# Performance work log

Hardware: AMD Instinct MI355X
Metric: run time of the kernel (lower is better)

Reference implementation:

```python
import jax, jax.numpy as jnp
import numpy as np

E, CAP, S, H, I, K = 160, 120, 3200, 2048, 192, 6  # experts, capacity, seq, hidden, per-device ffn dim, top-k


def setup_inputs() -> dict:
    key = jax.random.key(0)
    ks = jax.random.split(key, 8)
    hidden_states = jax.random.normal(ks[0], (S, H), jnp.float32)
    token_index = jax.random.randint(ks[1], (E, CAP), 0, S, dtype=jnp.int32)
    # re_index is a permutation mapping concatenated per-expert outputs back to (topk, seq) order
    re_index = jax.random.permutation(ks[2], E * CAP).astype(jnp.int32)
    topk_weight = jax.random.uniform(ks[3], (K, S, 1), jnp.float32)
    shared_out = jax.random.normal(ks[4], (1, S, H), jnp.float32)
    scale = 0.02
    gate_w = jax.random.normal(ks[5], (E, I, H), jnp.float32) * scale
    up_w = jax.random.normal(ks[6], (E, I, H), jnp.float32) * scale
    down_w = jax.random.normal(ks[7], (E, H, I), jnp.float32) * scale
    return {
        "hidden_states": hidden_states,
        "token_index": token_index,
        "re_index": re_index,
        "topk_weight": topk_weight,
        "shared_out": shared_out,
        "gate_w": gate_w,
        "up_w": up_w,
        "down_w": down_w,
    }


def reference(hidden_states, token_index, re_index, topk_weight, shared_out, gate_w, up_w, down_w):
    # Gather per-expert token groups: [E, CAP, H]
    x = hidden_states[token_index]
    # SwiGLU expert FFN, batched over all experts (grouped GEMM)
    g = jnp.einsum('ech,eih->eci', x, gate_w)   # [E, CAP, I]
    u = jnp.einsum('ech,eih->eci', x, up_w)     # [E, CAP, I]
    h = jax.nn.silu(g) * u
    o = jnp.einsum('eci,ehi->ech', h, down_w)   # [E, CAP, H]
    # Scatter back into (topk, seq) layout and combine with routing weights
    flat = o.reshape(E * CAP, H)[re_index].reshape(K, S, H)
    out = (flat * topk_weight).sum(axis=0, keepdims=True) + shared_out  # [1, S, H]
    return out
```

## Files before the change

### kernel.cpp

```cpp
#include <hip/hip_runtime.h>
#include <hip/hip_bf16.h>

#define E_ 160
#define CAP_ 120
#define S_ 3200
#define H_ 2048
#define I_ 192
#define K_ 6
#define MP_ 128

typedef __attribute__((ext_vector_type(8))) short short8;
typedef __attribute__((ext_vector_type(4))) float f32x4;

__device__ __forceinline__ unsigned pack2bf(float a, float b) {
  return __builtin_amdgcn_perm(__float_as_uint(b), __float_as_uint(a), 0x07060302u);
}
__device__ __forceinline__ short f2bf1(float a) {
  return (short)(__float_as_uint(a) >> 16);
}
__device__ __forceinline__ float bf2f(short s) {
  return __uint_as_float(((unsigned)(unsigned short)s) << 16);
}

__global__ __launch_bounds__(256) void k_gather(
    const float* __restrict__ hidden, const int* __restrict__ tok,
    short* __restrict__ xb)
{
  int b = blockIdx.x;
  int e = b >> 7, c = b & 127;
  int col = threadIdx.x * 8;
  short* dst = xb + (size_t)b * H_ + col;
  if (c < CAP_) {
    int row = tok[e * CAP_ + c];
    const float* src = hidden + (size_t)row * H_ + col;
    float4 f0 = *(const float4*)src;
    float4 f1 = *(const float4*)(src + 4);
    int4 v;
    v.x = (int)pack2bf(f0.x, f0.y); v.y = (int)pack2bf(f0.z, f0.w);
    v.z = (int)pack2bf(f1.x, f1.y); v.w = (int)pack2bf(f1.z, f1.w);
    *(int4*)dst = v;
  } else {
    *(int4*)dst = make_int4(0, 0, 0, 0);
  }
}

__global__ __launch_bounds__(256) void k_gateup(
    const short* __restrict__ xb, const float* __restrict__ gw,
    const float* __restrict__ uw, short* __restrict__ hb)
{
  __shared__ __align__(16) char smem[34816];
  short* As = (short*)smem;
  short* Bs = As + 128 * 64;

  int bid = blockIdx.x;
  int e = bid / 3, t = bid - e * 3;
  int i0 = t * 64;
  int tid = threadIdx.x;
  int lane = tid & 63, w = tid >> 6;
  int wr = w >> 1, wc = w & 1;
  int lrow = lane & 15, lq = lane >> 4;

  f32x4 acc[4][4] = {};
  const size_t xbase = (size_t)e * MP_ * H_;

  for (int kk = 0; kk < H_ / 64; ++kk) {
    int k0 = kk * 64;
#pragma unroll
    for (int r = 0; r < 4; ++r) {
      int q = r * 256 + tid;
      int row = q >> 3, cc = q & 7;
      int4 v = *(const int4*)(xb + xbase + (size_t)row * H_ + k0 + cc * 8);
      *(int4*)(As + row * 64 + cc * 8) = v;
    }
#pragma unroll
    for (int r = 0; r < 8; ++r) {
      int p = r * 256 + tid;
      int row = p >> 4, cc = p & 15;
      const float* srcw = (row < 64)
          ? (gw + ((size_t)e * I_ + i0 + row) * H_ + k0 + cc * 4)
          : (uw + ((size_t)e * I_ + i0 + row - 64) * H_ + k0 + cc * 4);
      float4 f = *(const float4*)srcw;
      uint2 pv;
      pv.x = pack2bf(f.x, f.y); pv.y = pack2bf(f.z, f.w);
      *(uint2*)(Bs + row * 64 + cc * 4) = pv;
    }
    __syncthreads();
#pragma unroll
    for (int ks = 0; ks < 2; ++ks) {
      int koff = ks * 32 + lq * 8;
      short8 a[4], bb[4];
#pragma unroll
      for (int tr = 0; tr < 4; ++tr)
        a[tr] = *(const short8*)(As + (wr * 64 + tr * 16 + lrow) * 64 + koff);
#pragma unroll
      for (int tc = 0; tc < 4; ++tc)
        bb[tc] = *(const short8*)(Bs + (wc * 64 + tc * 16 + lrow) * 64 + koff);
#pragma unroll
      for (int tr = 0; tr < 4; ++tr)
#pragma unroll
        for (int tc = 0; tc < 4; ++tc)
          acc[tr][tc] = __builtin_amdgcn_mfma_f32_16x16x32_bf16(
              a[tr], bb[tc], acc[tr][tc], 0, 0, 0);
    }
    __syncthreads();
  }

  float* exch = (float*)smem;
  if (wc == 0) {
#pragma unroll
    for (int tr = 0; tr < 4; ++tr)
#pragma unroll
      for (int tc = 0; tc < 4; ++tc)
#pragma unroll
        for (int rg = 0; rg < 4; ++rg) {
          int lr = tr * 16 + lq * 4 + rg;
          int lcol = tc * 16 + lrow;
          exch[(wr * 64 + lr) * 68 + lcol] = acc[tr][tc][rg];
        }
  }
  __syncthreads();
  if (wc == 1) {
#pragma unroll
    for (int tr = 0; tr < 4; ++tr)
#pragma unroll
      for (int tc = 0; tc < 4; ++tc)
#pragma unroll
        for (int rg = 0; rg < 4; ++rg) {
          int lr = tr * 16 + lq * 4 + rg;
          int lcol = tc * 16 + lrow;
          float g = exch[(wr * 64 + lr) * 68 + lcol];
          float u = acc[tr][tc][rg];
          float hv = g / (1.f + __expf(-g)) * u;
          hb[((size_t)e * MP_ + wr * 64 + lr) * I_ + i0 + lcol] = f2bf1(hv);
        }
  }
}

__global__ __launch_bounds__(256) void k_down(
    const short* __restrict__ hb, const float* __restrict__ dw,
    short* __restrict__ ob)
{
  __shared__ __align__(16) short As[128 * 64];
  __shared__ __align__(16) short Bs[128 * 64];
  int bid = blockIdx.x;
  int e = bid >> 4, t = bid & 15;
  int n0 = t * 128;
  int tid = threadIdx.x;
  int lane = tid & 63, w = tid >> 6;
  int wr = w >> 1, wc = w & 1;
  int lrow = lane & 15, lq = lane >> 4;

  f32x4 acc[4][4] = {};

  for (int kk = 0; kk < 3; ++kk) {
    int k0 = kk * 64;
#pragma unroll
    for (int r = 0; r < 4; ++r) {
      int q = r * 256 + tid;
      int row = q >> 3, cc = q & 7;
      int4 v = *(const int4*)(hb + ((size_t)e * MP_ + row) * I_ + k0 + cc * 8);
      *(int4*)(As + row * 64 + cc * 8) = v;
    }
#pragma unroll
    for (int r = 0; r < 8; ++r) {
      int p = r * 256 + tid;
      int row = p >> 4, cc = p & 15;
      const float* srcw = dw + ((size_t)e * H_ + n0 + row) * I_ + k0 + cc * 4;
      float4 f = *(const float4*)srcw;
      uint2 pv;
      pv.x = pack2bf(f.x, f.y); pv.y = pack2bf(f.z, f.w);
      *(uint2*)(Bs + row * 64 + cc * 4) = pv;
    }
    __syncthreads();
#pragma unroll
    for (int ks = 0; ks < 2; ++ks) {
      int koff = ks * 32 + lq * 8;
      short8 a[4], bb[4];
#pragma unroll
      for (int tr = 0; tr < 4; ++tr)
        a[tr] = *(const short8*)(As + (wr * 64 + tr * 16 + lrow) * 64 + koff);
#pragma unroll
      for (int tc = 0; tc < 4; ++tc)
        bb[tc] = *(const short8*)(Bs + (wc * 64 + tc * 16 + lrow) * 64 + koff);
#pragma unroll
      for (int tr = 0; tr < 4; ++tr)
#pragma unroll
        for (int tc = 0; tc < 4; ++tc)
          acc[tr][tc] = __builtin_amdgcn_mfma_f32_16x16x32_bf16(
              a[tr], bb[tc], acc[tr][tc], 0, 0, 0);
    }
    __syncthreads();
  }

#pragma unroll
  for (int tr = 0; tr < 4; ++tr) {
#pragma unroll
    for (int rg = 0; rg < 4; ++rg) {
      int c = wr * 64 + tr * 16 + lq * 4 + rg;
      if (c < CAP_) {
#pragma unroll
        for (int tc = 0; tc < 4; ++tc) {
          int col = n0 + wc * 64 + tc * 16 + lrow;
          ob[((size_t)e * CAP_ + c) * H_ + col] = f2bf1(acc[tr][tc][rg]);
        }
      }
    }
  }
}

__global__ __launch_bounds__(256) void k_combine(
    const short* __restrict__ ob, const int* __restrict__ re_index,
    const float* __restrict__ topk, const float* __restrict__ shared_out,
    float* __restrict__ out)
{
  int s = blockIdx.x;
  int c0 = threadIdx.x * 8;
  const float* sh = shared_out + (size_t)s * H_ + c0;
  float4 s0 = *(const float4*)sh;
  float4 s1 = *(const float4*)(sh + 4);
  float r[8] = {s0.x, s0.y, s0.z, s0.w, s1.x, s1.y, s1.z, s1.w};
#pragma unroll
  for (int k = 0; k < K_; ++k) {
    int p = k * S_ + s;
    int idx = re_index[p];
    float wgt = topk[p];
    const short* row = ob + (size_t)idx * H_ + c0;
    short8 v = *(const short8*)row;
#pragma unroll
    for (int j = 0; j < 8; ++j) r[j] += wgt * bf2f(v[j]);
  }
  float* o = out + (size_t)s * H_ + c0;
  float4 o0, o1;
  o0.x = r[0]; o0.y = r[1]; o0.z = r[2]; o0.w = r[3];
  o1.x = r[4]; o1.y = r[5]; o1.z = r[6]; o1.w = r[7];
  *(float4*)o = o0;
  *(float4*)(o + 4) = o1;
}

extern "C" void kernel_launch(void* const* d_in, const int* in_sizes, int n_in,
                              void* d_out, int out_size, void* d_ws, size_t ws_size,
                              hipStream_t stream) {
  const float* hidden     = (const float*)d_in[0];
  const int*   tok        = (const int*)d_in[1];
  const int*   re_index   = (const int*)d_in[2];
  const float* topk       = (const float*)d_in[3];
  const float* shared_out = (const float*)d_in[4];
  const float* gw         = (const float*)d_in[5];
  const float* uw         = (const float*)d_in[6];
  const float* dw         = (const float*)d_in[7];
  float* out = (float*)d_out;

  char* ws = (char*)d_ws;
  short* xb = (short*)ws;
  short* hb = (short*)(ws + (size_t)E_ * MP_ * H_ * 2);
  short* ob = (short*)(ws + (size_t)E_ * MP_ * H_ * 2
                          + (size_t)E_ * MP_ * I_ * 2);

  hipLaunchKernelGGL(k_gather,  dim3(E_ * MP_), dim3(256), 0, stream, hidden, tok, xb);
  hipLaunchKernelGGL(k_gateup,  dim3(E_ * 3),   dim3(256), 0, stream, xb, gw, uw, hb);
  hipLaunchKernelGGL(k_down,    dim3(E_ * 16),  dim3(256), 0, stream, hb, dw, ob);
  hipLaunchKernelGGL(k_combine, dim3(S_),       dim3(256), 0, stream, ob, re_index, topk, shared_out, out);
}
```

Baseline: 738.2 us.

## Fuse token gather into gate/up GEMM with register prefetch and swizzled LDS

Removes the separate gather kernel so the gate/up GEMM reads hidden rows directly by token index and converts them to bf16 on the fly. The gate/up tile is split along M (64 rows), doubling the grid to 960 blocks. Global loads for the next K step are prefetched into registers while the current step computes. Both GEMMs now use an XOR-swizzled LDS layout to reduce bank conflicts. The cost is that each weight tile is converted twice (once per M half) and hidden rows are re-read per i-tile.

```diff
diff --git a/kernel.cpp b/kernel.cpp
--- a/kernel.cpp
+++ b/kernel.cpp
@@ -21,117 +21,152 @@
 __device__ __forceinline__ float bf2f(short s) {
   return __uint_as_float(((unsigned)(unsigned short)s) << 16);
 }
-
-__global__ __launch_bounds__(256) void k_gather(
+__device__ __forceinline__ int4 pack8(float4 lo, float4 hi) {
+  int4 v;
+  v.x = (int)pack2bf(lo.x, lo.y); v.y = (int)pack2bf(lo.z, lo.w);
+  v.z = (int)pack2bf(hi.x, hi.y); v.w = (int)pack2bf(hi.z, hi.w);
+  return v;
+}
+
+#define NI_GU (H_ / 64)
+__global__ __launch_bounds__(256) void k_gateup(
     const float* __restrict__ hidden, const int* __restrict__ tok,
-    short* __restrict__ xb)
+    const float* __restrict__ gw, const float* __restrict__ uw,
+    short* __restrict__ hb)
 {
-  int b = blockIdx.x;
-  int e = b >> 7, c = b & 127;
-  int col = threadIdx.x * 8;
-  short* dst = xb + (size_t)b * H_ + col;
-  if (c < CAP_) {
-    int row = tok[e * CAP_ + c];
-    const float* src = hidden + (size_t)row * H_ + col;
-    float4 f0 = *(const float4*)src;
-    float4 f1 = *(const float4*)(src + 4);
-    int4 v;
-    v.x = (int)pack2bf(f0.x, f0.y); v.y = (int)pack2bf(f0.z, f0.w);
-    v.z = (int)pack2bf(f1.x, f1.y); v.w = (int)pack2bf(f1.z, f1.w);
-    *(int4*)dst = v;
-  } else {
-    *(int4*)dst = make_int4(0, 0, 0, 0);
-  }
-}
-
-__global__ __launch_bounds__(256) void k_gateup(
-    const short* __restrict__ xb, const float* __restrict__ gw,
-    const float* __restrict__ uw, short* __restrict__ hb)
-{
-  __shared__ __align__(16) char smem[34816];
+  __shared__ __align__(16) char smem[(64 * 64 + 128 * 64) * 2];
   short* As = (short*)smem;
-  short* Bs = As + 128 * 64;
+  short* Bs = As + 64 * 64;
 
   int bid = blockIdx.x;
-  int e = bid / 3, t = bid - e * 3;
-  int i0 = t * 64;
+  int e = bid / 6;
+  int r6 = bid - e * 6;
+  int it = r6 >> 1, mt = r6 & 1;
+  int i0 = it * 64, m0 = mt * 64;
   int tid = threadIdx.x;
   int lane = tid & 63, w = tid >> 6;
   int wr = w >> 1, wc = w & 1;
   int lrow = lane & 15, lq = lane >> 4;
 
-  f32x4 acc[4][4] = {};
-  const size_t xbase = (size_t)e * MP_ * H_;
-
-  for (int kk = 0; kk < H_ / 64; ++kk) {
-    int k0 = kk * 64;
-#pragma unroll
-    for (int r = 0; r < 4; ++r) {
-      int q = r * 256 + tid;
-      int row = q >> 3, cc = q & 7;
-      int4 v = *(const int4*)(xb + xbase + (size_t)row * H_ + k0 + cc * 8);
-      *(int4*)(As + row * 64 + cc * 8) = v;
-    }
-#pragma unroll
-    for (int r = 0; r < 8; ++r) {
-      int p = r * 256 + tid;
-      int row = p >> 4, cc = p & 15;
-      const float* srcw = (row < 64)
-          ? (gw + ((size_t)e * I_ + i0 + row) * H_ + k0 + cc * 4)
-          : (uw + ((size_t)e * I_ + i0 + row - 64) * H_ + k0 + cc * 4);
-      float4 f = *(const float4*)srcw;
-      uint2 pv;
-      pv.x = pack2bf(f.x, f.y); pv.y = pack2bf(f.z, f.w);
-      *(uint2*)(Bs + row * 64 + cc * 4) = pv;
-    }
-    __syncthreads();
+  const float* aptr[2]; int aphys[2];
+#pragma unroll
+  for (int q = 0; q < 2; ++q) {
+    int c = q * 256 + tid;
+    int arow = c >> 3, jc = c & 7;
+    int tr_ = m0 + arow; if (tr_ > CAP_ - 1) tr_ = CAP_ - 1;
+    int tokrow = tok[e * CAP_ + tr_];
+    aptr[q] = hidden + (size_t)tokrow * H_ + jc * 8;
+    aphys[q] = arow * 8 + (jc ^ (arow & 7));
+  }
+  const float* bptr[4]; int bphys[4];
+#pragma unroll
+  for (int q = 0; q < 4; ++q) {
+    int c = q * 256 + tid;
+    int brow = c >> 3, jc = c & 7;
+    const float* base = (brow < 64)
+        ? gw + ((size_t)e * I_ + i0 + brow) * H_
+        : uw + ((size_t)e * I_ + i0 + brow - 64) * H_;
+    bptr[q] = base + jc * 8;
+    bphys[q] = brow * 8 + (jc ^ (brow & 7));
+  }
+
+  f32x4 acc[2][4] = {};
+  float4 apre[2][2], bpre[4][2];
+
+#pragma unroll
+  for (int q = 0; q < 2; ++q) {
+    apre[q][0] = *(const float4*)(aptr[q]);
+    apre[q][1] = *(const float4*)(aptr[q] + 4);
+  }
+#pragma unroll
+  for (int q = 0; q < 4; ++q) {
+    bpre[q][0] = *(const float4*)(bptr[q]);
+    bpre[q][1] = *(const float4*)(bptr[q] + 4);
+  }
+#pragma unroll
+  for (int q = 0; q < 2; ++q)
+    *(int4*)(As + aphys[q] * 8) = pack8(apre[q][0], apre[q][1]);
+#pragma unroll
+  for (int q = 0; q < 4; ++q)
+    *(int4*)(Bs + bphys[q] * 8) = pack8(bpre[q][0], bpre[q][1]);
+  __syncthreads();
+
+  for (int kk = 0; kk < NI_GU; ++kk) {
+    bool hasNext = (kk + 1) < NI_GU;
+    if (hasNext) {
+      int k0 = (kk + 1) * 64;
+#pragma unroll
+      for (int q = 0; q < 2; ++q) {
+        apre[q][0] = *(const float4*)(aptr[q] + k0);
+        apre[q][1] = *(const float4*)(aptr[q] + k0 + 4);
+      }
+#pragma unroll
+      for (int q = 0; q < 4; ++q) {
+        bpre[q][0] = *(const float4*)(bptr[q] + k0);
+        bpre[q][1] = *(const float4*)(bptr[q] + k0 + 4);
+      }
+    }
 #pragma unroll
     for (int ks = 0; ks < 2; ++ks) {
-      int koff = ks * 32 + lq * 8;
-      short8 a[4], bb[4];
-#pragma unroll
-      for (int tr = 0; tr < 4; ++tr)
-        a[tr] = *(const short8*)(As + (wr * 64 + tr * 16 + lrow) * 64 + koff);
-#pragma unroll
-      for (int tc = 0; tc < 4; ++tc)
-        bb[tc] = *(const short8*)(Bs + (wc * 64 + tc * 16 + lrow) * 64 + koff);
-#pragma unroll
-      for (int tr = 0; tr < 4; ++tr)
+      short8 a[2], bb[4];
+#pragma unroll
+      for (int tr = 0; tr < 2; ++tr) {
+        int m = wr * 32 + tr * 16 + lrow;
+        int jc = ks * 4 + lq;
+        a[tr] = *(const short8*)(As + (m * 8 + (jc ^ (m & 7))) * 8);
+      }
+#pragma unroll
+      for (int tc = 0; tc < 4; ++tc) {
+        int n = wc * 64 + tc * 16 + lrow;
+        int jc = ks * 4 + lq;
+        bb[tc] = *(const short8*)(Bs + (n * 8 + (jc ^ (n & 7))) * 8);
+      }
+#pragma unroll
+      for (int tr = 0; tr < 2; ++tr)
 #pragma unroll
         for (int tc = 0; tc < 4; ++tc)
           acc[tr][tc] = __builtin_amdgcn_mfma_f32_16x16x32_bf16(
               a[tr], bb[tc], acc[tr][tc], 0, 0, 0);
     }
     __syncthreads();
+    if (hasNext) {
+#pragma unroll
+      for (int q = 0; q < 2; ++q)
+        *(int4*)(As + aphys[q] * 8) = pack8(apre[q][0], apre[q][1]);
+#pragma unroll
+      for (int q = 0; q < 4; ++q)
+        *(int4*)(Bs + bphys[q] * 8) = pack8(bpre[q][0], bpre[q][1]);
+    }
+    __syncthreads();
   }
 
   float* exch = (float*)smem;
   if (wc == 0) {
 #pragma unroll
-    for (int tr = 0; tr < 4; ++tr)
+    for (int tr = 0; tr < 2; ++tr)
 #pragma unroll
       for (int tc = 0; tc < 4; ++tc)
 #pragma unroll
         for (int rg = 0; rg < 4; ++rg) {
-          int lr = tr * 16 + lq * 4 + rg;
-          int lcol = tc * 16 + lrow;
-          exch[(wr * 64 + lr) * 68 + lcol] = acc[tr][tc][rg];
+          int row = wr * 32 + tr * 16 + lq * 4 + rg;
+          int col = tc * 16 + lrow;
+          exch[row * 68 + col] = acc[tr][tc][rg];
         }
   }
   __syncthreads();
   if (wc == 1) {
 #pragma unroll
-    for (int tr = 0; tr < 4; ++tr)
+    for (int tr = 0; tr < 2; ++tr)
 #pragma unroll
       for (int tc = 0; tc < 4; ++tc)
 #pragma unroll
         for (int rg = 0; rg < 4; ++rg) {
-          int lr = tr * 16 + lq * 4 + rg;
-          int lcol = tc * 16 + lrow;
-          float g = exch[(wr * 64 + lr) * 68 + lcol];
+          int row = wr * 32 + tr * 16 + lq * 4 + rg;
+          int col = tc * 16 + lrow;
+          float g = exch[row * 68 + col];
           float u = acc[tr][tc][rg];
           float hv = g / (1.f + __expf(-g)) * u;
-          hb[((size_t)e * MP_ + wr * 64 + lr) * I_ + i0 + lcol] = f2bf1(hv);
+          hb[((size_t)e * MP_ + m0 + row) * I_ + i0 + col] = f2bf1(hv);
         }
   }
 }
@@ -155,33 +190,37 @@
   for (int kk = 0; kk < 3; ++kk) {
     int k0 = kk * 64;
 #pragma unroll
-    for (int r = 0; r < 4; ++r) {
-      int q = r * 256 + tid;
-      int row = q >> 3, cc = q & 7;
-      int4 v = *(const int4*)(hb + ((size_t)e * MP_ + row) * I_ + k0 + cc * 8);
-      *(int4*)(As + row * 64 + cc * 8) = v;
-    }
-#pragma unroll
-    for (int r = 0; r < 8; ++r) {
-      int p = r * 256 + tid;
-      int row = p >> 4, cc = p & 15;
-      const float* srcw = dw + ((size_t)e * H_ + n0 + row) * I_ + k0 + cc * 4;
-      float4 f = *(const float4*)srcw;
-      uint2 pv;
-      pv.x = pack2bf(f.x, f.y); pv.y = pack2bf(f.z, f.w);
-      *(uint2*)(Bs + row * 64 + cc * 4) = pv;
+    for (int q = 0; q < 4; ++q) {
+      int c = q * 256 + tid;
+      int arow = c >> 3, jc = c & 7;
+      int4 v = *(const int4*)(hb + ((size_t)e * MP_ + arow) * I_ + k0 + jc * 8);
+      *(int4*)(As + (arow * 8 + (jc ^ (arow & 7))) * 8) = v;
+    }
+#pragma unroll
+    for (int q = 0; q < 4; ++q) {
+      int c = q * 256 + tid;
+      int brow = c >> 3, jc = c & 7;
+      const float* src = dw + ((size_t)e * H_ + n0 + brow) * I_ + k0 + jc * 8;
+      float4 lo = *(const float4*)src;
+      float4 hi = *(const float4*)(src + 4);
+      *(int4*)(Bs + (brow * 8 + (jc ^ (brow & 7))) * 8) = pack8(lo, hi);
     }
     __syncthreads();
 #pragma unroll
     for (int ks = 0; ks < 2; ++ks) {
-      int koff = ks * 32 + lq * 8;
       short8 a[4], bb[4];
 #pragma unroll
-      for (int tr = 0; tr < 4; ++tr)
-        a[tr] = *(const short8*)(As + (wr * 64 + tr * 16 + lrow) * 64 + koff);
-#pragma unroll
-      for (int tc = 0; tc < 4; ++tc)
-        bb[tc] = *(const short8*)(Bs + (wc * 64 + tc * 16 + lrow) * 64 + koff);
+      for (int tr = 0; tr < 4; ++tr) {
+        int m = wr * 64 + tr * 16 + lrow;
+        int jc = ks * 4 + lq;
+        a[tr] = *(const short8*)(As + (m * 8 + (jc ^ (m & 7))) * 8);
+      }
+#pragma unroll
+      for (int tc = 0; tc < 4; ++tc) {
+        int n = wc * 64 + tc * 16 + lrow;
+        int jc = ks * 4 + lq;
+        bb[tc] = *(const short8*)(Bs + (n * 8 + (jc ^ (n & 7))) * 8);
+      }
 #pragma unroll
       for (int tr = 0; tr < 4; ++tr)
 #pragma unroll
@@ -251,13 +290,12 @@
   float* out = (float*)d_out;
 
   char* ws = (char*)d_ws;
-  short* xb = (short*)ws;
-  short* hb = (short*)(ws + (size_t)E_ * MP_ * H_ * 2);
-  short* ob = (short*)(ws + (size_t)E_ * MP_ * H_ * 2
-                          + (size_t)E_ * MP_ * I_ * 2);
-
-  hipLaunchKernelGGL(k_gather,  dim3(E_ * MP_), dim3(256), 0, stream, hidden, tok, xb);
-  hipLaunchKernelGGL(k_gateup,  dim3(E_ * 3),   dim3(256), 0, stream, xb, gw, uw, hb);
-  hipLaunchKernelGGL(k_down,    dim3(E_ * 16),  dim3(256), 0, stream, hb, dw, ob);
-  hipLaunchKernelGGL(k_combine, dim3(S_),       dim3(256), 0, stream, ob, re_index, topk, shared_out, out);
-}
+  short* hb = (short*)ws;
+  short* ob = (short*)(ws + (size_t)E_ * MP_ * I_ * 2);
+
+  hipLaunchKernelGGL(k_gateup,  dim3(E_ * 6),  dim3(256), 0, stream,
+                     hidden, tok, gw, uw, hb);
+  hipLaunchKernelGGL(k_down,    dim3(E_ * 16), dim3(256), 0, stream, hb, dw, ob);
+  hipLaunchKernelGGL(k_combine, dim3(S_),      dim3(256), 0, stream,
+                     ob, re_index, topk, shared_out, out);
+}
```

Measured after the change: 775.9 us. 5.1% more time.
